# Performance work log

Hardware: AMD Instinct MI355X
Metric: run time of the kernel (lower is better)

## Reference

```python
import jax, jax.numpy as jnp
import numpy as np

B, T, D_MODEL, D_HEAD = 8, 2048, 1024, 64


def setup_inputs() -> dict:
    key = jax.random.key(0)
    kx, kq, kk, kv = jax.random.split(key, 4)
    s = 1.0 / np.sqrt(D_MODEL)
    return {
        "x": jax.random.normal(kx, (B, T, D_MODEL), dtype=jnp.float32),
        "W_Q": jax.random.normal(kq, (D_MODEL, D_HEAD), dtype=jnp.float32) * s,
        "W_K": jax.random.normal(kk, (D_MODEL, D_HEAD), dtype=jnp.float32) * s,
        "W_V": jax.random.normal(kv, (D_MODEL, D_HEAD), dtype=jnp.float32) * s,
    }


def reference(x, W_Q, W_K, W_V):
    # x: [B, T, d_model]; projections -> [B, T, d_head]
    q = jnp.einsum("btd,dh->bth", x, W_Q)
    k = jnp.einsum("btd,dh->bth", x, W_K)
    v = jnp.einsum("btd,dh->bth", x, W_V)
    d_head = W_Q.shape[-1]
    scale = 1.0 / jnp.sqrt(jnp.asarray(d_head, dtype=x.dtype))
    # scores: [B, T, T], causal mask (lower-triangular kept)
    scores = jnp.einsum("bqh,bkh->bqk", q, k) * scale
    T_ = x.shape[1]
    causal = jnp.tril(jnp.ones((T_, T_), dtype=bool))
    scores = jnp.where(causal[None, :, :], scores, jnp.asarray(-jnp.inf, dtype=x.dtype))
    a = jax.nn.softmax(scores, axis=-1)
    # dropout omitted (eval mode / identity)
    out = jnp.einsum("bqk,bkh->bqh", a, v)
    return out
```

## Files before the change

### kernel.cpp

```cpp
#include <hip/hip_runtime.h>

#define TT   2048
#define DM   1024
#define DH   64
#define NB   8
#define BK   128
#define KST  72

typedef __attribute__((ext_vector_type(4))) float          f32x4;
typedef __attribute__((ext_vector_type(4))) int            i32x4;
typedef __attribute__((ext_vector_type(4))) unsigned short u16x4;
typedef __attribute__((ext_vector_type(8))) short          s16x8;

__device__ __forceinline__ unsigned short f2bf(float f) {
  unsigned int u = __float_as_uint(f);
  u += 0x7fffu + ((u >> 16) & 1u);
  return (unsigned short)(u >> 16);
}

#define MFMA(acc, a, b) \
  (acc) = __builtin_amdgcn_mfma_f32_16x16x32_bf16((a), (b), (acc), 0, 0, 0)

__device__ __forceinline__ void gload_lds16(const void* g, void* l) {
  __builtin_amdgcn_global_load_lds(
      (const __attribute__((address_space(1))) void*)g,
      (__attribute__((address_space(3))) void*)l, 16, 0, 0);
}

#define WS_WT    0u
#define WS_QK    393216u
#define WS_VT    4587520u
#define WS_OP    6684672u
#define WS_ML    16121856u

__global__ __launch_bounds__(256) void pack_w_kernel(
    const float* __restrict__ wq, const float* __restrict__ wk,
    const float* __restrict__ wv, unsigned short* __restrict__ wt) {
  int idx = blockIdx.x * 256 + threadIdx.x;
  if (idx >= 192 * DM) return;
  int n = idx >> 10;
  int k = idx & (DM - 1);
  const float* src = (n < 64) ? wq : ((n < 128) ? wk : wv);
  wt[(size_t)n * DM + k] = f2bf(src[(size_t)k * DH + (n & 63)]);
}

__global__ __launch_bounds__(256) void qkv_gemm_kernel(
    const float* __restrict__ x, const unsigned short* __restrict__ wt,
    unsigned short* __restrict__ qkvqk, unsigned short* __restrict__ vt) {
  __shared__ __align__(16) float          a_lds[32 * BK];
  __shared__ __align__(16) unsigned short b_lds[192 * BK];

  const int tid  = threadIdx.x;
  const int lane = tid & 63;
  const int w    = tid >> 6;
  const int ln   = lane & 15;
  const int quad = lane >> 4;
  const int mw   = w & 1;
  const int nw   = w >> 1;
  const int m0   = blockIdx.x * 32;
  const int n0   = nw * 96;
  const int lsw  = ln & 7;

  int agoff[4];
  #pragma unroll
  for (int i = 0; i < 4; ++i) {
    int s = i * 256 + w * 64 + lane;
    int m = s >> 5, cc = s & 31;
    agoff[i] = (m0 + m) * DM + ((cc ^ (m & 7)) << 2);
  }
  int bgoff[12];
  #pragma unroll
  for (int j = 0; j < 12; ++j) {
    int s = j * 256 + w * 64 + lane;
    int n = s >> 4, cc = s & 15;
    bgoff[j] = n * DM + ((cc ^ (n & 7)) << 3);
  }

  f32x4 acc[6];
  #pragma unroll
  for (int i = 0; i < 6; ++i) acc[i] = (f32x4){0.f, 0.f, 0.f, 0.f};
  union { s16x8 v; unsigned short h[8]; } ap;

  #pragma unroll
  for (int i = 0; i < 4; ++i)
    gload_lds16(x + agoff[i], (void*)(a_lds + (i * 256 + w * 64) * 4));
  #pragma unroll
  for (int j = 0; j < 12; ++j)
    gload_lds16(wt + bgoff[j], (void*)(b_lds + (j * 256 + w * 64) * 8));

  for (int k0 = 0; k0 < DM; k0 += BK) {
    __syncthreads();
    #pragma unroll
    for (int ks = 0; ks < BK; ks += 32) {
      const int m  = mw * 16 + ln;
      const int c0 = (ks >> 2) + 2 * quad;
      f32x4 v0 = *(const f32x4*)&a_lds[m * BK + ((c0 ^ lsw) << 2)];
      f32x4 v1 = *(const f32x4*)&a_lds[m * BK + (((c0 + 1) ^ lsw) << 2)];
      #pragma unroll
      for (int j = 0; j < 4; ++j) { ap.h[j] = f2bf(v0[j]); ap.h[4 + j] = f2bf(v1[j]); }
      s16x8 af = ap.v;
      const int cb = (ks >> 3) + quad;
      #pragma unroll
      for (int nt = 0; nt < 6; ++nt) {
        int n = n0 + nt * 16 + ln;
        s16x8 bf = *(const s16x8*)&b_lds[n * BK + ((cb ^ lsw) << 3)];
        MFMA(acc[nt], af, bf);
      }
    }
    __syncthreads();
    if (k0 + BK < DM) {
      const int kn = k0 + BK;
      #pragma unroll
      for (int i = 0; i < 4; ++i)
        gload_lds16(x + agoff[i] + kn, (void*)(a_lds + (i * 256 + w * 64) * 4));
      #pragma unroll
      for (int j = 0; j < 12; ++j)
        gload_lds16(wt + bgoff[j] + kn, (void*)(b_lds + (j * 256 + w * 64) * 8));
    }
  }

  const float QS = 0.18033688011112042f;
  const int mm0 = m0 + mw * 16;
  const int bz  = mm0 >> 11;
  const int tb  = (mm0 & 2047) + quad * 4;
  #pragma unroll
  for (int nt = 0; nt < 6; ++nt) {
    const int ncol = n0 + nt * 16 + ln;
    if (ncol < 128) {
      const float sc = (ncol < 64) ? QS : 1.0f;
      #pragma unroll
      for (int r = 0; r < 4; ++r) {
        int row = mm0 + quad * 4 + r;
        qkvqk[(size_t)row * 128 + ncol] = f2bf(acc[nt][r] * sc);
      }
    } else {
      int d = ncol - 128;
      u16x4 h;
      #pragma unroll
      for (int r = 0; r < 4; ++r) h[r] = f2bf(acc[nt][r]);
      *(u16x4*)(vt + ((size_t)bz * 64 + d) * TT + tb) = h;
    }
  }
}

__global__ __launch_bounds__(256) void attn_part_kernel(
    const unsigned short* __restrict__ qkvqk, const unsigned short* __restrict__ vt,
    unsigned short* __restrict__ opart, float* __restrict__ ml) {
  const int Ctab[16] = {0,1,2,4,6,9,12,16,20,25,30,36,42,49,56,64};
  const int f  = blockIdx.x;
  const int bz = f / 72;
  const int rw = f - bz * 72;
  int s = 0;
  #pragma unroll
  for (int t = 1; t < 16; ++t) if (rw >= Ctab[t]) s = t;
  const int c = rw - Ctab[s];
  const int ntiles = min(4, 2 * s + 2 - 4 * c);
  const int qtA = 2 * s, qtB = 2 * s + 1;

  __shared__ __align__(16) unsigned short k_lds[256 * 64];
  __shared__ __align__(16) unsigned short v_lds[64 * 256];
  __shared__ __align__(16) unsigned short p_lds[64 * KST];

  const int tid  = threadIdx.x;
  const int w    = tid >> 6;
  const int lane = tid & 63;
  const int ln   = lane & 15;
  const int quad = lane >> 4;
  const int lsw  = ln & 7;
  const int bb   = bz * TT;
  const int kbase = c * 256;

  #pragma unroll
  for (int i = 0; i < 8; ++i) {
    int base = (i * 4 + w) * 64;
    int slot = base + lane;
    int row = slot >> 3, cc = slot & 7;
    gload_lds16(qkvqk + (size_t)(bb + kbase + row) * 128 + 64 + ((cc ^ (row & 7)) << 3),
                (void*)(k_lds + base * 8));
  }
  #pragma unroll
  for (int i = 0; i < 8; ++i) {
    int base = (i * 4 + w) * 64;
    int slot = base + lane;
    int d = slot >> 5, cc = slot & 31;
    gload_lds16(vt + ((size_t)bz * 64 + d) * TT + kbase + ((cc ^ (d & 7)) << 3),
                (void*)(v_lds + base * 8));
  }

  const unsigned short* qrowA = qkvqk + (size_t)(bb + qtA * 64 + w * 16 + ln) * 128;
  const unsigned short* qrowB = qrowA + 64 * 128;
  const s16x8 qfA0 = *(const s16x8*)(qrowA + quad * 8);
  const s16x8 qfA1 = *(const s16x8*)(qrowA + 32 + quad * 8);
  const s16x8 qfB0 = *(const s16x8*)(qrowB + quad * 8);
  const s16x8 qfB1 = *(const s16x8*)(qrowB + 32 + quad * 8);

  s16x8 ones;
  #pragma unroll
  for (int j = 0; j < 8; ++j) ones[j] = (short)0x3F80;

  f32x4 acc_oA[4], acc_oB[4], acc_lA, acc_lB;
  #pragma unroll
  for (int i = 0; i < 4; ++i) {
    acc_oA[i] = (f32x4){0.f, 0.f, 0.f, 0.f};
    acc_oB[i] = (f32x4){0.f, 0.f, 0.f, 0.f};
  }
  acc_lA = (f32x4){0.f, 0.f, 0.f, 0.f};
  acc_lB = (f32x4){0.f, 0.f, 0.f, 0.f};

  const int qgA = qtA * 64 + w * 16 + quad * 4;
  const int qgB = qgA + 64;
  __syncthreads();

  for (int ct = 0; ct < ntiles; ++ct) {
    const int ktg = c * 4 + ct;
    const int kc0 = quad;
    const int kc1 = 4 + quad;

    if (ktg <= qtA) {
      const bool diag = (ktg == qtA);
      f32x4 acc_s[4];
      #pragma unroll
      for (int i = 0; i < 4; ++i) acc_s[i] = (f32x4){0.f, 0.f, 0.f, 0.f};
      #pragma unroll
      for (int ns = 0; ns < 4; ++ns) {
        const int krow = ct * 64 + ns * 16 + ln;
        s16x8 kf0 = *(const s16x8*)&k_lds[krow * 64 + ((kc0 ^ lsw) << 3)];
        s16x8 kf1 = *(const s16x8*)&k_lds[krow * 64 + ((kc1 ^ lsw) << 3)];
        MFMA(acc_s[ns], qfA0, kf0);
        MFMA(acc_s[ns], qfA1, kf1);
      }
      #pragma unroll
      for (int r = 0; r < 4; ++r) {
        const int qg = qgA + r;
        #pragma unroll
        for (int ns = 0; ns < 4; ++ns) {
          float sv = acc_s[ns][r];
          if (diag) {
            int kg = ktg * 64 + ns * 16 + ln;
            sv = (kg <= qg) ? sv : -1e30f;
          }
          p_lds[(w * 16 + quad * 4 + r) * KST + ns * 16 + ln] = f2bf(exp2f(sv));
        }
      }
      #pragma unroll
      for (int kk = 0; kk < 64; kk += 32) {
        s16x8 pf = *(const s16x8*)&p_lds[(w * 16 + ln) * KST + kk + quad * 8];
        MFMA(acc_lA, pf, ones);
        #pragma unroll
        for (int nt = 0; nt < 4; ++nt) {
          const int d  = nt * 16 + ln;
          const int sc = ct * 8 + (((kk >> 3) + quad) ^ lsw);
          s16x8 vf = *(const s16x8*)&v_lds[d * 256 + sc * 8];
          MFMA(acc_oA[nt], pf, vf);
        }
      }
      asm volatile("" ::: "memory");
    }

    {
      const bool diag = (ktg == qtB);
      f32x4 acc_s[4];
      #pragma unroll
      for (int i = 0; i < 4; ++i) acc_s[i] = (f32x4){0.f, 0.f, 0.f, 0.f};
      #pragma unroll
      for (int ns = 0; ns < 4; ++ns) {
        const int krow = ct * 64 + ns * 16 + ln;
        s16x8 kf0 = *(const s16x8*)&k_lds[krow * 64 + ((kc0 ^ lsw) << 3)];
        s16x8 kf1 = *(const s16x8*)&k_lds[krow * 64 + ((kc1 ^ lsw) << 3)];
        MFMA(acc_s[ns], qfB0, kf0);
        MFMA(acc_s[ns], qfB1, kf1);
      }
      #pragma unroll
      for (int r = 0; r < 4; ++r) {
        const int qg = qgB + r;
        #pragma unroll
        for (int ns = 0; ns < 4; ++ns) {
          float sv = acc_s[ns][r];
          if (diag) {
            int kg = ktg * 64 + ns * 16 + ln;
            sv = (kg <= qg) ? sv : -1e30f;
          }
          p_lds[(w * 16 + quad * 4 + r) * KST + ns * 16 + ln] = f2bf(exp2f(sv));
        }
      }
      #pragma unroll
      for (int kk = 0; kk < 64; kk += 32) {
        s16x8 pf = *(const s16x8*)&p_lds[(w * 16 + ln) * KST + kk + quad * 8];
        MFMA(acc_lB, pf, ones);
        #pragma unroll
        for (int nt = 0; nt < 4; ++nt) {
          const int d  = nt * 16 + ln;
          const int sc = ct * 8 + (((kk >> 3) + quad) ^ lsw);
          s16x8 vf = *(const s16x8*)&v_lds[d * 256 + sc * 8];
          MFMA(acc_oB[nt], pf, vf);
        }
      }
      asm volatile("" ::: "memory");
    }
  }

  #pragma unroll
  for (int half = 0; half < 2; ++half) {
    const int qt = (half == 0) ? qtA : qtB;
    const int g  = qt >> 2, rq = qt & 3;
    const int base = qt + 2 * g * (g - 1) + rq * g;
    const size_t slab = (size_t)bz * 144 + base + c;
    unsigned short* op = opart + slab * 4096;
    const f32x4* ao = (half == 0) ? acc_oA : acc_oB;
    const f32x4  al = (half == 0) ? acc_lA : acc_lB;
    #pragma unroll
    for (int nt = 0; nt < 4; ++nt)
      #pragma unroll
      for (int r = 0; r < 4; ++r)
        op[(w * 16 + quad * 4 + r) * 64 + nt * 16 + ln] = f2bf(ao[nt][r]);
    if (ln == 0) {
      float* lp = ml + slab * 64;
      #pragma unroll
      for (int r = 0; r < 4; ++r)
        lp[w * 16 + quad * 4 + r] = al[r];
    }
  }
}

__global__ __launch_bounds__(256) void attn_combine_kernel(
    const unsigned short* __restrict__ opart, const float* __restrict__ ml,
    float* __restrict__ out) {
  const int qt = blockIdx.x;
  const int bz = blockIdx.y;
  const int aq = qt >> 2, rq = qt & 3;
  const int nch = aq + 1;
  const int base = qt + 2 * aq * (aq - 1) + rq * aq;
  const size_t slab0 = (size_t)bz * 144 + base;

  const int tid = threadIdx.x;
  const int row = tid >> 2;
  const int ds  = (tid & 3) * 16;

  float L = 0.f;
  float acc[16];
  #pragma unroll
  for (int j = 0; j < 16; ++j) acc[j] = 0.f;
  #pragma unroll 8
  for (int ch = 0; ch < nch; ++ch) {
    L += ml[(slab0 + ch) * 64 + row];
    const unsigned short* op = opart + (slab0 + ch) * 4096 + row * 64 + ds;
    i32x4 v0 = *(const i32x4*)(op);
    i32x4 v1 = *(const i32x4*)(op + 8);
    #pragma unroll
    for (int j = 0; j < 4; ++j) {
      unsigned int u0 = (unsigned int)v0[j], u1 = (unsigned int)v1[j];
      acc[j * 2]         += __uint_as_float(u0 << 16);
      acc[j * 2 + 1]     += __uint_as_float(u0 & 0xffff0000u);
      acc[8 + j * 2]     += __uint_as_float(u1 << 16);
      acc[8 + j * 2 + 1] += __uint_as_float(u1 & 0xffff0000u);
    }
  }
  float inv = 1.0f / L;
  float* o = out + ((size_t)bz * TT + qt * 64 + row) * 64 + ds;
  #pragma unroll
  for (int j = 0; j < 16; ++j) o[j] = acc[j] * inv;
}

extern "C" void kernel_launch(void* const* d_in, const int* in_sizes, int n_in,
                              void* d_out, int out_size, void* d_ws, size_t ws_size,
                              hipStream_t stream) {
  const float* x  = (const float*)d_in[0];
  const float* wq = (const float*)d_in[1];
  const float* wk = (const float*)d_in[2];
  const float* wv = (const float*)d_in[3];
  float* out = (float*)d_out;

  char* ws = (char*)d_ws;
  unsigned short* wt    = (unsigned short*)(ws + WS_WT);
  unsigned short* qkvqk = (unsigned short*)(ws + WS_QK);
  unsigned short* vt    = (unsigned short*)(ws + WS_VT);
  unsigned short* opart = (unsigned short*)(ws + WS_OP);
  float*          ml    = (float*)(ws + WS_ML);

  pack_w_kernel<<<(192 * DM + 255) / 256, 256, 0, stream>>>(wq, wk, wv, wt);
  qkv_gemm_kernel<<<NB * TT / 32, 256, 0, stream>>>(x, wt, qkvqk, vt);
  attn_part_kernel<<<NB * 72, 256, 0, stream>>>(qkvqk, vt, opart, ml);
  attn_combine_kernel<<<dim3(32, NB), 256, 0, stream>>>(opart, ml, out);
}
```

Baseline: 138.2 us.

## Read K and V fragments directly from global memory instead of staging in LDS

Removes the 64 KB K/V shared-memory staging and the block barrier in the attention partial kernel. Each wave now loads its K and V MFMA fragments straight from global memory (via cache), and launch bounds request 3 blocks per CU to raise occupancy now that LDS use is small. This trades cooperative LDS reuse across the four waves for redundant, less coalesced global/L2 traffic. Each K/V element is now read by every wave and for both query tiles.

```diff
diff --git a/kernel.cpp b/kernel.cpp
--- a/kernel.cpp
+++ b/kernel.cpp
@@ -143,7 +143,7 @@
   }
 }
 
-__global__ __launch_bounds__(256) void attn_part_kernel(
+__global__ __launch_bounds__(256, 3) void attn_part_kernel(
     const unsigned short* __restrict__ qkvqk, const unsigned short* __restrict__ vt,
     unsigned short* __restrict__ opart, float* __restrict__ ml) {
   const int Ctab[16] = {0,1,2,4,6,9,12,16,20,25,30,36,42,49,56,64};
@@ -157,8 +157,6 @@
   const int ntiles = min(4, 2 * s + 2 - 4 * c);
   const int qtA = 2 * s, qtB = 2 * s + 1;
 
-  __shared__ __align__(16) unsigned short k_lds[256 * 64];
-  __shared__ __align__(16) unsigned short v_lds[64 * 256];
   __shared__ __align__(16) unsigned short p_lds[64 * KST];
 
   const int tid  = threadIdx.x;
@@ -166,26 +164,11 @@
   const int lane = tid & 63;
   const int ln   = lane & 15;
   const int quad = lane >> 4;
-  const int lsw  = ln & 7;
   const int bb   = bz * TT;
   const int kbase = c * 256;
 
-  #pragma unroll
-  for (int i = 0; i < 8; ++i) {
-    int base = (i * 4 + w) * 64;
-    int slot = base + lane;
-    int row = slot >> 3, cc = slot & 7;
-    gload_lds16(qkvqk + (size_t)(bb + kbase + row) * 128 + 64 + ((cc ^ (row & 7)) << 3),
-                (void*)(k_lds + base * 8));
-  }
-  #pragma unroll
-  for (int i = 0; i < 8; ++i) {
-    int base = (i * 4 + w) * 64;
-    int slot = base + lane;
-    int d = slot >> 5, cc = slot & 31;
-    gload_lds16(vt + ((size_t)bz * 64 + d) * TT + kbase + ((cc ^ (d & 7)) << 3),
-                (void*)(v_lds + base * 8));
-  }
+  const unsigned short* kp = qkvqk + (size_t)(bb + kbase) * 128 + 64 + quad * 8;
+  const unsigned short* vp = vt + (size_t)bz * 64 * TT + kbase + quad * 8;
 
   const unsigned short* qrowA = qkvqk + (size_t)(bb + qtA * 64 + w * 16 + ln) * 128;
   const unsigned short* qrowB = qrowA + 64 * 128;
@@ -209,12 +192,9 @@
 
   const int qgA = qtA * 64 + w * 16 + quad * 4;
   const int qgB = qgA + 64;
-  __syncthreads();
 
   for (int ct = 0; ct < ntiles; ++ct) {
     const int ktg = c * 4 + ct;
-    const int kc0 = quad;
-    const int kc1 = 4 + quad;
 
     if (ktg <= qtA) {
       const bool diag = (ktg == qtA);
@@ -224,8 +204,9 @@
       #pragma unroll
       for (int ns = 0; ns < 4; ++ns) {
         const int krow = ct * 64 + ns * 16 + ln;
-        s16x8 kf0 = *(const s16x8*)&k_lds[krow * 64 + ((kc0 ^ lsw) << 3)];
-        s16x8 kf1 = *(const s16x8*)&k_lds[krow * 64 + ((kc1 ^ lsw) << 3)];
+        const unsigned short* krp = kp + (size_t)krow * 128;
+        s16x8 kf0 = *(const s16x8*)(krp);
+        s16x8 kf1 = *(const s16x8*)(krp + 32);
         MFMA(acc_s[ns], qfA0, kf0);
         MFMA(acc_s[ns], qfA1, kf1);
       }
@@ -248,9 +229,8 @@
         MFMA(acc_lA, pf, ones);
         #pragma unroll
         for (int nt = 0; nt < 4; ++nt) {
-          const int d  = nt * 16 + ln;
-          const int sc = ct * 8 + (((kk >> 3) + quad) ^ lsw);
-          s16x8 vf = *(const s16x8*)&v_lds[d * 256 + sc * 8];
+          const int d = nt * 16 + ln;
+          s16x8 vf = *(const s16x8*)(vp + (size_t)d * TT + ct * 64 + kk);
           MFMA(acc_oA[nt], pf, vf);
         }
       }
@@ -265,8 +245,9 @@
       #pragma unroll
       for (int ns = 0; ns < 4; ++ns) {
         const int krow = ct * 64 + ns * 16 + ln;
-        s16x8 kf0 = *(const s16x8*)&k_lds[krow * 64 + ((kc0 ^ lsw) << 3)];
-        s16x8 kf1 = *(const s16x8*)&k_lds[krow * 64 + ((kc1 ^ lsw) << 3)];
+        const unsigned short* krp = kp + (size_t)krow * 128;
+        s16x8 kf0 = *(const s16x8*)(krp);
+        s16x8 kf1 = *(const s16x8*)(krp + 32);
         MFMA(acc_s[ns], qfB0, kf0);
         MFMA(acc_s[ns], qfB1, kf1);
       }
@@ -289,9 +270,8 @@
         MFMA(acc_lB, pf, ones);
         #pragma unroll
         for (int nt = 0; nt < 4; ++nt) {
-          const int d  = nt * 16 + ln;
-          const int sc = ct * 8 + (((kk >> 3) + quad) ^ lsw);
-          s16x8 vf = *(const s16x8*)&v_lds[d * 256 + sc * 8];
+          const int d = nt * 16 + ln;
+          s16x8 vf = *(const s16x8*)(vp + (size_t)d * TT + ct * 64 + kk);
           MFMA(acc_oB[nt], pf, vf);
         }
       }
```

Measured after the change: 162.4 us. +17.5%, slower.
